# Kernel tuning notes

Hardware: AMD Instinct MI355X
Metric: run time of the kernel (lower is better)

## Reference

```python
import jax, jax.numpy as jnp
import numpy as np

N_NODES = 50000
N_EDGES = 1600000
NODE_DIM = 16
EDGE_DIM = 16
PIPE_F = 4
HID = 64
L = 3


def _lin(k, fan_in, fan_out):
    kw, kb = jax.random.split(k)
    bound = 1.0 / np.sqrt(fan_in)
    w = jax.random.uniform(kw, (fan_in, fan_out), jnp.float32, -bound, bound)
    b = jax.random.uniform(kb, (fan_out,), jnp.float32, -bound, bound)
    return w, b


def setup_inputs() -> dict:
    key = jax.random.key(0)
    ks = jax.random.split(key, 16)
    leak_area = jax.random.normal(ks[0], (N_NODES, 1), jnp.float32)
    pipe_attrs = jax.random.normal(ks[1], (N_EDGES, PIPE_F), jnp.float32)
    edge_index = jax.random.randint(ks[2], (2, N_EDGES), 0, N_NODES, jnp.int32)
    node_embed_w, node_embed_b = _lin(ks[3], 1, NODE_DIM)
    edge_embed_w, edge_embed_b = _lin(ks[4], PIPE_F, EDGE_DIM)
    # per-layer MLP params, stacked along leading layer axis
    ew1, eb1, ew2, eb2, nw1, nb1, nw2, nb2 = [], [], [], [], [], [], [], []
    for l in range(L):
        kl = jax.random.fold_in(ks[5], l)
        k1, k2, k3, k4 = jax.random.split(kl, 4)
        w, b = _lin(k1, 2 * NODE_DIM + EDGE_DIM, HID); ew1.append(w); eb1.append(b)
        w, b = _lin(k2, HID, EDGE_DIM); ew2.append(w); eb2.append(b)
        w, b = _lin(k3, NODE_DIM + EDGE_DIM, HID); nw1.append(w); nb1.append(b)
        w, b = _lin(k4, HID, NODE_DIM); nw2.append(w); nb2.append(b)
    final_node_w, final_node_b = _lin(ks[6], NODE_DIM, 1)
    final_edge_w, final_edge_b = _lin(ks[7], EDGE_DIM, 1)
    return {
        "leak_area": leak_area,
        "pipe_attrs": pipe_attrs,
        "edge_index": edge_index,
        "node_embed_w": node_embed_w, "node_embed_b": node_embed_b,
        "edge_embed_w": edge_embed_w, "edge_embed_b": edge_embed_b,
        "edge_mlp_w1": jnp.stack(ew1), "edge_mlp_b1": jnp.stack(eb1),
        "edge_mlp_w2": jnp.stack(ew2), "edge_mlp_b2": jnp.stack(eb2),
        "node_mlp_w1": jnp.stack(nw1), "node_mlp_b1": jnp.stack(nb1),
        "node_mlp_w2": jnp.stack(nw2), "node_mlp_b2": jnp.stack(nb2),
        "final_node_w": final_node_w, "final_node_b": final_node_b,
        "final_edge_w": final_edge_w, "final_edge_b": final_edge_b,
    }


def reference(leak_area, pipe_attrs, edge_index,
              node_embed_w, node_embed_b, edge_embed_w, edge_embed_b,
              edge_mlp_w1, edge_mlp_b1, edge_mlp_w2, edge_mlp_b2,
              node_mlp_w1, node_mlp_b1, node_mlp_w2, node_mlp_b2,
              final_node_w, final_node_b, final_edge_w, final_edge_b):
    x = leak_area @ node_embed_w + node_embed_b          # [N, node_dim]
    e = pipe_attrs @ edge_embed_w + edge_embed_b          # [E, edge_dim]
    src = edge_index[0]  # x_j (source, PyG default flow source_to_target)
    dst = edge_index[1]  # x_i (target); aggregation index
    n = x.shape[0]
    num_layers = edge_mlp_w1.shape[0]
    ones = jnp.ones((src.shape[0], 1), x.dtype)
    deg = jax.ops.segment_sum(ones, dst, num_segments=n)  # [N,1]
    inv_deg = 1.0 / jnp.maximum(deg, 1.0)
    for l in range(num_layers):
        # message: small MLP on [x_i, x_j, e] per edge
        m_in = jnp.concatenate([x[dst], x[src], e], axis=-1)       # [E, 2d+de]
        h = jax.nn.relu(m_in @ edge_mlp_w1[l] + edge_mlp_b1[l])    # [E, 64]
        msg = h @ edge_mlp_w2[l] + edge_mlp_b2[l]                  # [E, de]
        # mean-aggregate to target nodes
        aggr = jax.ops.segment_sum(msg, dst, num_segments=n) * inv_deg  # [N, de]
        # node update MLP
        u_in = jnp.concatenate([x, aggr], axis=-1)                 # [N, d+de]
        x = jax.nn.relu(u_in @ node_mlp_w1[l] + node_mlp_b1[l]) @ node_mlp_w2[l] + node_mlp_b2[l]
    H = (x @ final_node_w + final_node_b)[:, 0]   # [N]
    q = (e @ final_edge_w + final_edge_b)[:, 0]   # [E]
    return H, q
```

## Files before the change

### kernel.cpp

```cpp
#include <hip/hip_runtime.h>
#include <hip/hip_bf16.h>

#define NN 50000
#define NE 1600000
#define NB 391
#define CBLK 392
#define EPB 4096

typedef __attribute__((ext_vector_type(8))) short bf16x8;
typedef __attribute__((ext_vector_type(4))) float f32x4;

#define B_HAG   0
#define B_QW    (B_HAG + NN*64*4)
#define B_NF    (B_QW + 32)
#define B_W1B   (B_NF + 3*8*64*8*2)
#define B_XB0   (B_W1B + 3*8*64*8*2)
#define B_XB1   (B_XB0 + NN*16*2)
#define B_EPK   (B_XB1 + NN*16*2)
#define B_OFF   (B_EPK + NE*16)
#define B_BCNT  (B_OFF + (NN+1)*4)
#define B_BASE  (B_BCNT + CBLK*NB*4)
#define B_GTOT  (B_BASE + (NB+1)*4)
#define B_END   (B_GTOT + NB*4)

static __device__ __forceinline__ unsigned short f2bf(float f) {
    union { __hip_bfloat16 h; unsigned short u; } cv;
    cv.h = __float2bfloat16(f);
    return cv.u;
}
static __device__ __forceinline__ unsigned pk2(float a, float b) {
    unsigned r;
    asm("v_cvt_pk_bf16_f32 %0, %1, %2" : "=v"(r) : "v"(a), "v"(b));
    return r;
}
static __device__ __forceinline__ float bf2f(unsigned short u) {
    return __uint_as_float((unsigned)u << 16);
}
static __device__ __forceinline__ bf16x8 mk8(unsigned a, unsigned b, unsigned c, unsigned d) {
    union { bf16x8 v; uint4 u; } cv;
    cv.u = make_uint4(a, b, c, d);
    return cv.v;
}

__global__ __launch_bounds__(1024) void fused_init_kernel(
    const float* __restrict__ ew1, const float* __restrict__ eb1,
    const float* __restrict__ nw1, const float* __restrict__ ew2,
    const float* __restrict__ nw2,
    const float* __restrict__ eeW, const float* __restrict__ eeB,
    const float* __restrict__ few, const float* __restrict__ feb,
    unsigned short* __restrict__ w1b, unsigned short* __restrict__ nf,
    float* __restrict__ qw,
    const float* __restrict__ leak, const float* __restrict__ ne_w,
    const float* __restrict__ ne_b,
    unsigned short* __restrict__ xb0, float* __restrict__ hag,
    const int* __restrict__ dst, int* __restrict__ bcnt)
{
    __shared__ int hist[NB];
    int t = threadIdx.x;
    for (int i = t; i < NB; i += 1024) hist[i] = 0;
    __syncthreads();
    int base = blockIdx.x * EPB;
    int b[4];
    #pragma unroll
    for (int i = 0; i < 4; i++) {
        int idx = base + i * 1024 + t;
        b[i] = (idx < NE) ? (dst[idx] >> 7) : -1;
    }
    #pragma unroll
    for (int i = 0; i < 4; i++)
        if (b[i] >= 0) atomicAdd(&hist[b[i]], 1);

    int gtid = blockIdx.x * 1024 + t;
    int gstride = CBLK * 1024;
    for (int idx = gtid; idx < 3 * 8 * 64 * 8; idx += gstride) {
        int l = idx >> 12;
        int r = idx & 4095;
        int f = r >> 9;
        int lane = (r >> 3) & 63;
        int e = r & 7;
        int col = lane & 15;
        int krow = ((lane >> 4) << 3) + e;
        {
            int tt = f >> 1, s = f & 1;
            int k = krow + (s << 5);
            int j = (tt << 4) + col;
            float v = 0.f;
            if (k < 32) {
                v = ew1[l * 3072 + k * 64 + j];
            } else if (k < 36) {
                int f2 = k - 32;
                float acc = 0.f;
                for (int m = 0; m < 16; m++) acc += eeW[f2 * 16 + m] * ew1[l * 3072 + (32 + m) * 64 + j];
                v = acc;
            } else if (k == 36) {
                float acc = eb1[l * 64 + j];
                for (int m = 0; m < 16; m++) acc += eeB[m] * ew1[l * 3072 + (32 + m) * 64 + j];
                v = acc;
            }
            w1b[idx] = f2bf(v);
        }
        {
            float v;
            if (f < 2)      v = ew2[l * 1024 + (f * 32 + krow) * 16 + col];
            else if (f < 6) v = nw1[l * 2048 + krow * 64 + (f - 2) * 16 + col];
            else            v = nw2[l * 1024 + ((f - 6) * 32 + krow) * 16 + col];
            nf[idx] = f2bf(v);
        }
    }
    if (gtid < 4) {
        float s = 0.f;
        for (int k = 0; k < 16; k++) s += eeW[gtid * 16 + k] * few[k];
        qw[gtid] = s;
    } else if (gtid == 4) {
        float s = feb[0];
        for (int k = 0; k < 16; k++) s += eeB[k] * few[k];
        qw[4] = s;
    }
    if (gtid < NN) {
        int n = gtid;
        float la = leak[n];
        float v[16];
        #pragma unroll
        for (int i = 0; i < 16; i++) v[i] = la * ne_w[i] + ne_b[i];
        unsigned pk[8];
        #pragma unroll
        for (int i = 0; i < 8; i++) pk[i] = pk2(v[2 * i], v[2 * i + 1]);
        uint4* xo = reinterpret_cast<uint4*>(xb0 + (size_t)n * 16);
        xo[0] = make_uint4(pk[0], pk[1], pk[2], pk[3]);
        xo[1] = make_uint4(pk[4], pk[5], pk[6], pk[7]);
        float4 z = {0.f, 0.f, 0.f, 0.f};
        float4* hp = reinterpret_cast<float4*>(hag + (size_t)n * 64);
        #pragma unroll
        for (int j = 0; j < 16; j++) hp[j] = z;
    }

    __syncthreads();
    for (int i = t; i < NB; i += 1024) bcnt[blockIdx.x * NB + i] = hist[i];
}

__global__ __launch_bounds__(512) void scan_blocks_kernel(
    int* __restrict__ bcnt, int* __restrict__ gtot)
{
    __shared__ int sm[512];
    int b = blockIdx.x;
    int t = threadIdx.x;
    int v = (t < CBLK) ? bcnt[t * NB + b] : 0;
    sm[t] = v;
    __syncthreads();
    for (int o = 1; o < 512; o <<= 1) {
        int x = (t >= o) ? sm[t - o] : 0;
        __syncthreads();
        sm[t] += x;
        __syncthreads();
    }
    if (t < CBLK) bcnt[t * NB + b] = sm[t] - v;
    if (t == 511) gtot[b] = sm[511];
}

__global__ __launch_bounds__(512) void scan_top_kernel(
    const int* __restrict__ gtot, int* __restrict__ gbase)
{
    __shared__ int sm[512];
    int t = threadIdx.x;
    int v = (t < NB) ? gtot[t] : 0;
    sm[t] = v;
    __syncthreads();
    for (int o = 1; o < 512; o <<= 1) {
        int x = (t >= o) ? sm[t - o] : 0;
        __syncthreads();
        sm[t] += x;
        __syncthreads();
    }
    if (t < NB) gbase[t] = sm[t] - v;
    if (t == 0) gbase[NB] = NE;
}

__global__ __launch_bounds__(1024) void bucket_scatter_kernel(
    const int* __restrict__ ei, const float* __restrict__ pa,
    const int* __restrict__ bcnt, const int* __restrict__ gbase,
    const float* __restrict__ qw,
    float* __restrict__ qout, uint4* __restrict__ epk)
{
    __shared__ int hist[NB];
    int t = threadIdx.x;
    for (int i = t; i < NB; i += 1024) hist[i] = 0;
    __syncthreads();
    int base = blockIdx.x * EPB;
    float q0 = qw[0], q1 = qw[1], q2 = qw[2], q3 = qw[3], q4 = qw[4];
    int d[4], s[4];
    float4 p[4];
    #pragma unroll
    for (int i = 0; i < 4; i++) {
        int idx = base + i * 1024 + t;
        if (idx < NE) {
            d[i] = ei[NE + idx];
            s[i] = ei[idx];
            p[i] = reinterpret_cast<const float4*>(pa)[idx];
        } else {
            d[i] = -1;
        }
    }
    #pragma unroll
    for (int i = 0; i < 4; i++) {
        int idx = base + i * 1024 + t;
        if (d[i] >= 0)
            qout[idx] = q4 + p[i].x * q0 + p[i].y * q1 + p[i].z * q2 + p[i].w * q3;
    }
    int lr[4];
    #pragma unroll
    for (int i = 0; i < 4; i++)
        if (d[i] >= 0) lr[i] = atomicAdd(&hist[d[i] >> 7], 1);
    int bs[4];
    #pragma unroll
    for (int i = 0; i < 4; i++)
        if (d[i] >= 0) {
            int b = d[i] >> 7;
            bs[i] = gbase[b] + bcnt[blockIdx.x * NB + b];
        }
    #pragma unroll
    for (int i = 0; i < 4; i++)
        if (d[i] >= 0) {
            uint4 v;
            v.x = (unsigned)s[i];
            v.y = (unsigned)d[i];
            v.z = pk2(p[i].x, p[i].y);
            v.w = pk2(p[i].z, p[i].w);
            epk[bs[i] + lr[i]] = v;
        }
}

__global__ __launch_bounds__(1024) void fine_sort_kernel(
    const int* __restrict__ gbase, uint4* __restrict__ epk, int* __restrict__ off)
{
    __shared__ int hist[128];
    __shared__ int fb[128];
    int t = threadIdx.x;
    int b = blockIdx.x;
    int S = gbase[b], E = gbase[b + 1];
    if (t < 128) hist[t] = 0;
    __syncthreads();

    uint4 r[12];
    #pragma unroll
    for (int i = 0; i < 12; i++) {
        int gi = S + i * 1024 + t;
        if (gi < E) r[i] = epk[gi];
    }
    int lr[12];
    #pragma unroll
    for (int i = 0; i < 12; i++) {
        int gi = S + i * 1024 + t;
        if (gi < E) lr[i] = atomicAdd(&hist[(int)(r[i].y & 127u)], 1);
    }
    __syncthreads();
    if (t < 128) fb[t] = hist[t];
    __syncthreads();
    for (int o = 1; o < 128; o <<= 1) {
        int v = 0;
        if (t < 128 && t >= o) v = fb[t - o];
        __syncthreads();
        if (t < 128) fb[t] += v;
        __syncthreads();
    }
    int d0 = b << 7;
    if (t < 128 && d0 + t < NN) off[d0 + t] = S + fb[t] - hist[t];
    if (b == NB - 1 && t == 0) off[NN] = NE;
    __syncthreads();
    #pragma unroll
    for (int i = 0; i < 12; i++) {
        int gi = S + i * 1024 + t;
        if (gi < E) {
            int fd = (int)(r[i].y & 127u);
            int pos = S + (fb[fd] - hist[fd]) + lr[i];
            epk[pos] = r[i];
        }
    }
}

__global__ __launch_bounds__(128, 5) void edge_mfma_kernel(
    const unsigned short* __restrict__ xb,
    const uint4* __restrict__ epk,
    const int* __restrict__ off,
    const unsigned short* __restrict__ w1b,
    float* __restrict__ hag)
{
    __shared__ unsigned short hbuf[2][64 * 68];
    int tid = threadIdx.x;
    int lane = tid & 63;
    int wid = tid >> 6;
    int wave = blockIdx.x * 2 + wid;
    int base = wave * 64;
    if (base >= NE) return;
    int ar = lane & 15;
    int ap = lane >> 4;
    unsigned short* hb = &hbuf[wid][0];

    uint4 ev0 = epk[base + 0  + ar];
    uint4 ev1 = epk[base + 16 + ar];
    uint4 ev2 = epk[base + 32 + ar];
    uint4 ev3 = epk[base + 48 + ar];

    int r0 = (ap < 2) ? (int)ev0.y : (int)ev0.x;
    int r1 = (ap < 2) ? (int)ev1.y : (int)ev1.x;
    int r2 = (ap < 2) ? (int)ev2.y : (int)ev2.x;
    int r3 = (ap < 2) ? (int)ev3.y : (int)ev3.x;
    int half = (ap & 1) * 8;
    bf16x8 a00 = *reinterpret_cast<const bf16x8*>(xb + (size_t)r0 * 16 + half);
    bf16x8 a01 = *reinterpret_cast<const bf16x8*>(xb + (size_t)r1 * 16 + half);
    bf16x8 a02 = *reinterpret_cast<const bf16x8*>(xb + (size_t)r2 * 16 + half);
    bf16x8 a03 = *reinterpret_cast<const bf16x8*>(xb + (size_t)r3 * 16 + half);

    int d0 = __builtin_amdgcn_readfirstlane((int)ev0.y);

    bf16x8 Bf[8];
    const bf16x8* w1v = reinterpret_cast<const bf16x8*>(w1b);
    #pragma unroll
    for (int i = 0; i < 8; i++) Bf[i] = w1v[i * 64 + lane];

#define DO_TILE(EV, A0, TILE) do {                                             \
    bf16x8 a1 = (bf16x8)0;                                                     \
    if (ap == 0) {                                                             \
        a1[0] = (short)(EV.z & 0xffffu);                                       \
        a1[1] = (short)(EV.z >> 16);                                           \
        a1[2] = (short)(EV.w & 0xffffu);                                       \
        a1[3] = (short)(EV.w >> 16);                                           \
        a1[4] = (short)0x3f80;                                                 \
    }                                                                          \
    f32x4 C0 = {0.f, 0.f, 0.f, 0.f}, C1 = C0, C2 = C0, C3 = C0;                \
    C0 = __builtin_amdgcn_mfma_f32_16x16x32_bf16(A0, Bf[0], C0, 0, 0, 0);      \
    C0 = __builtin_amdgcn_mfma_f32_16x16x32_bf16(a1, Bf[1], C0, 0, 0, 0);      \
    C1 = __builtin_amdgcn_mfma_f32_16x16x32_bf16(A0, Bf[2], C1, 0, 0, 0);      \
    C1 = __builtin_amdgcn_mfma_f32_16x16x32_bf16(a1, Bf[3], C1, 0, 0, 0);      \
    C2 = __builtin_amdgcn_mfma_f32_16x16x32_bf16(A0, Bf[4], C2, 0, 0, 0);      \
    C2 = __builtin_amdgcn_mfma_f32_16x16x32_bf16(a1, Bf[5], C2, 0, 0, 0);      \
    C3 = __builtin_amdgcn_mfma_f32_16x16x32_bf16(A0, Bf[6], C3, 0, 0, 0);      \
    C3 = __builtin_amdgcn_mfma_f32_16x16x32_bf16(a1, Bf[7], C3, 0, 0, 0);      \
    int eoff = TILE * 16 + ap * 4;                                             \
    {                                                                          \
        unsigned lov = pk2(fmaxf(C0[0], 0.f), fmaxf(C0[1], 0.f));              \
        unsigned hiv = pk2(fmaxf(C0[2], 0.f), fmaxf(C0[3], 0.f));              \
        *reinterpret_cast<uint2*>(hb + (0 * 16 + ar) * 68 + eoff) = make_uint2(lov, hiv); \
    }                                                                          \
    {                                                                          \
        unsigned lov = pk2(fmaxf(C1[0], 0.f), fmaxf(C1[1], 0.f));              \
        unsigned hiv = pk2(fmaxf(C1[2], 0.f), fmaxf(C1[3], 0.f));              \
        *reinterpret_cast<uint2*>(hb + (1 * 16 + ar) * 68 + eoff) = make_uint2(lov, hiv); \
    }                                                                          \
    {                                                                          \
        unsigned lov = pk2(fmaxf(C2[0], 0.f), fmaxf(C2[1], 0.f));              \
        unsigned hiv = pk2(fmaxf(C2[2], 0.f), fmaxf(C2[3], 0.f));              \
        *reinterpret_cast<uint2*>(hb + (2 * 16 + ar) * 68 + eoff) = make_uint2(lov, hiv); \
    }                                                                          \
    {                                                                          \
        unsigned lov = pk2(fmaxf(C3[0], 0.f), fmaxf(C3[1], 0.f));              \
        unsigned hiv = pk2(fmaxf(C3[2], 0.f), fmaxf(C3[3], 0.f));              \
        *reinterpret_cast<uint2*>(hb + (3 * 16 + ar) * 68 + eoff) = make_uint2(lov, hiv); \
    }                                                                          \
} while (0)

    DO_TILE(ev0, a00, 0);
    DO_TILE(ev1, a01, 1);
    DO_TILE(ev2, a02, 2);
    DO_TILE(ev3, a03, 3);
#undef DO_TILE

    asm volatile("s_waitcnt lgkmcnt(0)" ::: "memory");
    __builtin_amdgcn_sched_barrier(0);

    int offd0 = off[d0];
    int d = d0;
    int e = base;
    const int lim = base + 64;
    const unsigned short* hr = hb + lane * 68;
    while (e < lim) {
        int segend = off[d + 1];
        int eend = segend < lim ? segend : lim;
        float acc = 0.f;
        int i = e - base, iend = eend - base;
        for (; (i & 3) != 0 && i < iend; ++i) acc += bf2f(hr[i]);
        for (; i + 4 <= iend; i += 4) {
            uint2 u = *reinterpret_cast<const uint2*>(hr + i);
            acc += __uint_as_float(u.x << 16) + __uint_as_float(u.x & 0xffff0000u)
                 + __uint_as_float(u.y << 16) + __uint_as_float(u.y & 0xffff0000u);
        }
        for (; i < iend; ++i) acc += bf2f(hr[i]);
        bool interior = (segend <= lim) && (e > base || offd0 == base);
        if (interior)
            hag[(size_t)d * 64 + lane] = acc;
        else
            unsafeAtomicAdd(&hag[(size_t)d * 64 + lane], acc);
        e = eend;
        if (segend <= lim) ++d;
    }
}

__global__ __launch_bounds__(256) void node_mfma_kernel(
    const unsigned short* __restrict__ xb, unsigned short* __restrict__ xbn,
    float* __restrict__ hag, const int* __restrict__ off,
    const unsigned short* __restrict__ nf,
    const float* __restrict__ eb2,
    const float* __restrict__ nb1, const float* __restrict__ nb2,
    const float* __restrict__ fnw, const float* __restrict__ fnb,
    float* __restrict__ Hout, int writeH)
{
    __shared__ unsigned short aggt[4][16 * 16];
    __shared__ unsigned short ht[4][16 * 64];
    __shared__ float ot[4][16 * 16];
    int tid = threadIdx.x;
    int lane = tid & 63;
    int wid = tid >> 6;
    int wave = blockIdx.x * 4 + wid;
    int n0 = wave * 16;
    if (n0 >= NN) return;
    int nr = lane & 15;
    int ap = lane >> 4;

    bf16x8 Bf[8];
    const bf16x8* nfv = reinterpret_cast<const bf16x8*>(nf);
    #pragma unroll
    for (int i = 0; i < 8; i++) Bf[i] = nfv[i * 64 + lane];

    float* hrow = hag + (size_t)(n0 + nr) * 64 + ap * 8;
    float4* h0p = reinterpret_cast<float4*>(hrow);
    float4* h1p = reinterpret_cast<float4*>(hrow + 32);
    float4 ha = h0p[0], hc = h0p[1];
    float4 he = h1p[0], hg = h1p[1];
    float4 z = {0.f, 0.f, 0.f, 0.f};
    h0p[0] = z; h0p[1] = z; h1p[0] = z; h1p[1] = z;
    bf16x8 agA0 = mk8(pk2(ha.x, ha.y), pk2(ha.z, ha.w), pk2(hc.x, hc.y), pk2(hc.z, hc.w));
    bf16x8 agA1 = mk8(pk2(he.x, he.y), pk2(he.z, he.w), pk2(hg.x, hg.y), pk2(hg.z, hg.w));
    f32x4 Cag = {0.f, 0.f, 0.f, 0.f};
    Cag = __builtin_amdgcn_mfma_f32_16x16x32_bf16(agA0, Bf[0], Cag, 0, 0, 0);
    Cag = __builtin_amdgcn_mfma_f32_16x16x32_bf16(agA1, Bf[1], Cag, 0, 0, 0);

    int bn = n0 + ap * 4;
    int o0 = off[bn], o1 = off[bn + 1], o2 = off[bn + 2], o3 = off[bn + 3], o4 = off[bn + 4];
    float ebv = eb2[nr];
    {
        int dgs[4] = {o1 - o0, o2 - o1, o3 - o2, o4 - o3};
        #pragma unroll
        for (int r = 0; r < 4; r++) {
            float inv = 1.0f / (float)(dgs[r] > 0 ? dgs[r] : 1);
            float val = Cag[r] * inv + ((dgs[r] > 0) ? ebv : 0.f);
            aggt[wid][(ap * 4 + r) * 16 + nr] = f2bf(val);
        }
    }
    asm volatile("s_waitcnt lgkmcnt(0)" ::: "memory");
    __builtin_amdgcn_sched_barrier(0);

    bf16x8 uA;
    if (ap < 2) uA = *reinterpret_cast<const bf16x8*>(xb + (size_t)(n0 + nr) * 16 + ap * 8);
    else        uA = *reinterpret_cast<const bf16x8*>(&aggt[wid][nr * 16 + (ap - 2) * 8]);

    f32x4 Ch0 = {0.f, 0.f, 0.f, 0.f}, Ch1 = Ch0, Ch2 = Ch0, Ch3 = Ch0;
    Ch0 = __builtin_amdgcn_mfma_f32_16x16x32_bf16(uA, Bf[2], Ch0, 0, 0, 0);
    Ch1 = __builtin_amdgcn_mfma_f32_16x16x32_bf16(uA, Bf[3], Ch1, 0, 0, 0);
    Ch2 = __builtin_amdgcn_mfma_f32_16x16x32_bf16(uA, Bf[4], Ch2, 0, 0, 0);
    Ch3 = __builtin_amdgcn_mfma_f32_16x16x32_bf16(uA, Bf[5], Ch3, 0, 0, 0);

#define H_EPI(C, TT) do {                                                      \
    int j = (TT) * 16 + nr;                                                    \
    float bv = nb1[j];                                                         \
    _Pragma("unroll")                                                          \
    for (int r = 0; r < 4; r++) {                                              \
        float h = fmaxf(C[r] + bv, 0.f);                                       \
        ht[wid][(ap * 4 + r) * 64 + j] = f2bf(h);                              \
    }                                                                          \
} while (0)
    H_EPI(Ch0, 0); H_EPI(Ch1, 1); H_EPI(Ch2, 2); H_EPI(Ch3, 3);
#undef H_EPI

    asm volatile("s_waitcnt lgkmcnt(0)" ::: "memory");
    __builtin_amdgcn_sched_barrier(0);

    bf16x8 hA0 = *reinterpret_cast<const bf16x8*>(&ht[wid][nr * 64 + ap * 8]);
    bf16x8 hA1 = *reinterpret_cast<const bf16x8*>(&ht[wid][nr * 64 + 32 + ap * 8]);
    f32x4 Co = {0.f, 0.f, 0.f, 0.f};
    Co = __builtin_amdgcn_mfma_f32_16x16x32_bf16(hA0, Bf[6], Co, 0, 0, 0);
    Co = __builtin_amdgcn_mfma_f32_16x16x32_bf16(hA1, Bf[7], Co, 0, 0, 0);
    {
        float bv = nb2[nr];
        #pragma unroll
        for (int r = 0; r < 4; r++) ot[wid][(ap * 4 + r) * 16 + nr] = Co[r] + bv;
    }
    asm volatile("s_waitcnt lgkmcnt(0)" ::: "memory");
    __builtin_amdgcn_sched_barrier(0);

    if (lane < 16) {
        const float* orow = &ot[wid][lane * 16];
        float o[16];
        #pragma unroll
        for (int k = 0; k < 16; k++) o[k] = orow[k];
        unsigned pk[8];
        #pragma unroll
        for (int i = 0; i < 8; i++) pk[i] = pk2(o[2 * i], o[2 * i + 1]);
        uint4* xo = reinterpret_cast<uint4*>(xbn + (size_t)(n0 + lane) * 16);
        xo[0] = make_uint4(pk[0], pk[1], pk[2], pk[3]);
        xo[1] = make_uint4(pk[4], pk[5], pk[6], pk[7]);
        if (writeH) {
            float s = fnb[0];
            #pragma unroll
            for (int k = 0; k < 16; k++) s += o[k] * fnw[k];
            Hout[n0 + lane] = s;
        }
    }
}

extern "C" void kernel_launch(void* const* d_in, const int* in_sizes, int n_in,
                              void* d_out, int out_size, void* d_ws, size_t ws_size,
                              hipStream_t stream)
{
    const float* leak = (const float*)d_in[0];
    const float* pa   = (const float*)d_in[1];
    const int*   ei   = (const int*)d_in[2];
    const float* neww = (const float*)d_in[3];
    const float* newb = (const float*)d_in[4];
    const float* eeW  = (const float*)d_in[5];
    const float* eeB  = (const float*)d_in[6];
    const float* ew1  = (const float*)d_in[7];
    const float* eb1  = (const float*)d_in[8];
    const float* ew2  = (const float*)d_in[9];
    const float* eb2  = (const float*)d_in[10];
    const float* nw1  = (const float*)d_in[11];
    const float* nb1  = (const float*)d_in[12];
    const float* nw2  = (const float*)d_in[13];
    const float* nb2  = (const float*)d_in[14];
    const float* fnw  = (const float*)d_in[15];
    const float* fnb  = (const float*)d_in[16];
    const float* few  = (const float*)d_in[17];
    const float* feb  = (const float*)d_in[18];

    char* wsb = (char*)d_ws;
    float*          hag   = (float*)(wsb + B_HAG);
    float*          qw    = (float*)(wsb + B_QW);
    unsigned short* nf    = (unsigned short*)(wsb + B_NF);
    unsigned short* w1b   = (unsigned short*)(wsb + B_W1B);
    unsigned short* xb0   = (unsigned short*)(wsb + B_XB0);
    unsigned short* xb1   = (unsigned short*)(wsb + B_XB1);
    uint4*          epk   = (uint4*)(wsb + B_EPK);
    int*            off   = (int*)(wsb + B_OFF);
    int*            bcnt  = (int*)(wsb + B_BCNT);
    int*            gbase = (int*)(wsb + B_BASE);
    int*            gtot  = (int*)(wsb + B_GTOT);

    float* H = (float*)d_out;
    float* q = (float*)d_out + NN;
    const int* dstp = ei + NE;

    fused_init_kernel<<<CBLK, 1024, 0, stream>>>(
        ew1, eb1, nw1, ew2, nw2, eeW, eeB, few, feb, w1b, nf, qw,
        leak, neww, newb, xb0, hag, dstp, bcnt);
    scan_blocks_kernel<<<NB, 512, 0, stream>>>(bcnt, gtot);
    scan_top_kernel<<<1, 512, 0, stream>>>(gtot, gbase);
    bucket_scatter_kernel<<<CBLK, 1024, 0, stream>>>(ei, pa, bcnt, gbase, qw, q, epk);
    fine_sort_kernel<<<NB, 1024, 0, stream>>>(gbase, epk, off);

    int nwaves = NN / 16;
    int nblocks = (nwaves + 3) / 4;

    unsigned short* xcur = xb0;
    unsigned short* xnxt = xb1;
    for (int l = 0; l < 3; l++) {
        edge_mfma_kernel<<<NE / 128, 128, 0, stream>>>(
            xcur, epk, off, w1b + l * 4096, hag);
        node_mfma_kernel<<<nblocks, 256, 0, stream>>>(
            xcur, xnxt, hag, off, nf + l * 4096, eb2 + l * 16,
            nb1 + l * 64, nb2 + l * 16, fnw, fnb, H, (l == 2) ? 1 : 0);
        unsigned short* tmp = xcur; xcur = xnxt; xnxt = tmp;
    }
}
```

Before: 202.2 us.

## Halve edge-kernel LDS staging by processing two 32-edge halves and raise occupancy

The edge MFMA kernel now stages hidden activations for only 32 edges at a time, cutting per-wave LDS from 64x68 to 64x36 shorts. It runs the segment-sum epilogue twice, once per half, and raises the launch-bounds occupancy hint from 5 to 8 blocks. The aim is more resident waves to hide gather latency. In exchange, every segment write is now an atomic add, including interior ones that were plain stores before, and segments crossing the half boundary produce extra atomics and off[] reads.

```diff
diff --git a/kernel.cpp b/kernel.cpp
--- a/kernel.cpp
+++ b/kernel.cpp
@@ -277,14 +277,14 @@
     }
 }
 
-__global__ __launch_bounds__(128, 5) void edge_mfma_kernel(
+__global__ __launch_bounds__(128, 8) void edge_mfma_kernel(
     const unsigned short* __restrict__ xb,
     const uint4* __restrict__ epk,
     const int* __restrict__ off,
     const unsigned short* __restrict__ w1b,
     float* __restrict__ hag)
 {
-    __shared__ unsigned short hbuf[2][64 * 68];
+    __shared__ unsigned short hbuf[2][64 * 36];
     int tid = threadIdx.x;
     int lane = tid & 63;
     int wid = tid >> 6;
@@ -317,7 +317,7 @@
     #pragma unroll
     for (int i = 0; i < 8; i++) Bf[i] = w1v[i * 64 + lane];
 
-#define DO_TILE(EV, A0, TILE) do {                                             \
+#define DO_TILE(EV, A0, HT) do {                                               \
     bf16x8 a1 = (bf16x8)0;                                                     \
     if (ap == 0) {                                                             \
         a1[0] = (short)(EV.z & 0xffffu);                                       \
@@ -335,63 +335,66 @@
     C2 = __builtin_amdgcn_mfma_f32_16x16x32_bf16(a1, Bf[5], C2, 0, 0, 0);      \
     C3 = __builtin_amdgcn_mfma_f32_16x16x32_bf16(A0, Bf[6], C3, 0, 0, 0);      \
     C3 = __builtin_amdgcn_mfma_f32_16x16x32_bf16(a1, Bf[7], C3, 0, 0, 0);      \
-    int eoff = TILE * 16 + ap * 4;                                             \
+    int eoff = (HT) * 16 + ap * 4;                                             \
     {                                                                          \
         unsigned lov = pk2(fmaxf(C0[0], 0.f), fmaxf(C0[1], 0.f));              \
         unsigned hiv = pk2(fmaxf(C0[2], 0.f), fmaxf(C0[3], 0.f));              \
-        *reinterpret_cast<uint2*>(hb + (0 * 16 + ar) * 68 + eoff) = make_uint2(lov, hiv); \
+        *reinterpret_cast<uint2*>(hb + (0 * 16 + ar) * 36 + eoff) = make_uint2(lov, hiv); \
     }                                                                          \
     {                                                                          \
         unsigned lov = pk2(fmaxf(C1[0], 0.f), fmaxf(C1[1], 0.f));              \
         unsigned hiv = pk2(fmaxf(C1[2], 0.f), fmaxf(C1[3], 0.f));              \
-        *reinterpret_cast<uint2*>(hb + (1 * 16 + ar) * 68 + eoff) = make_uint2(lov, hiv); \
+        *reinterpret_cast<uint2*>(hb + (1 * 16 + ar) * 36 + eoff) = make_uint2(lov, hiv); \
     }                                                                          \
     {                                                                          \
         unsigned lov = pk2(fmaxf(C2[0], 0.f), fmaxf(C2[1], 0.f));              \
         unsigned hiv = pk2(fmaxf(C2[2], 0.f), fmaxf(C2[3], 0.f));              \
-        *reinterpret_cast<uint2*>(hb + (2 * 16 + ar) * 68 + eoff) = make_uint2(lov, hiv); \
+        *reinterpret_cast<uint2*>(hb + (2 * 16 + ar) * 36 + eoff) = make_uint2(lov, hiv); \
     }                                                                          \
     {                                                                          \
         unsigned lov = pk2(fmaxf(C3[0], 0.f), fmaxf(C3[1], 0.f));              \
         unsigned hiv = pk2(fmaxf(C3[2], 0.f), fmaxf(C3[3], 0.f));              \
-        *reinterpret_cast<uint2*>(hb + (3 * 16 + ar) * 68 + eoff) = make_uint2(lov, hiv); \
+        *reinterpret_cast<uint2*>(hb + (3 * 16 + ar) * 36 + eoff) = make_uint2(lov, hiv); \
+    }                                                                          \
+} while (0)
+
+#define EPILOGUE(HSTART, HLIM) do {                                            \
+    const unsigned short* hr = hb + lane * 36;                                 \
+    while (e < (HLIM)) {                                                       \
+        int segend = off[d + 1];                                               \
+        int eend = segend < (HLIM) ? segend : (HLIM);                          \
+        float acc = 0.f;                                                       \
+        int i = e - (HSTART), iend = eend - (HSTART);                          \
+        for (; (i & 3) != 0 && i < iend; ++i) acc += bf2f(hr[i]);              \
+        for (; i + 4 <= iend; i += 4) {                                        \
+            uint2 u = *reinterpret_cast<const uint2*>(hr + i);                 \
+            acc += __uint_as_float(u.x << 16) + __uint_as_float(u.x & 0xffff0000u) \
+                 + __uint_as_float(u.y << 16) + __uint_as_float(u.y & 0xffff0000u); \
+        }                                                                      \
+        for (; i < iend; ++i) acc += bf2f(hr[i]);                              \
+        unsafeAtomicAdd(&hag[(size_t)d * 64 + lane], acc);                     \
+        e = eend;                                                              \
+        if (segend <= (HLIM)) ++d;                                             \
     }                                                                          \
 } while (0)
 
     DO_TILE(ev0, a00, 0);
     DO_TILE(ev1, a01, 1);
-    DO_TILE(ev2, a02, 2);
-    DO_TILE(ev3, a03, 3);
-#undef DO_TILE
-
     asm volatile("s_waitcnt lgkmcnt(0)" ::: "memory");
     __builtin_amdgcn_sched_barrier(0);
-
-    int offd0 = off[d0];
     int d = d0;
     int e = base;
-    const int lim = base + 64;
-    const unsigned short* hr = hb + lane * 68;
-    while (e < lim) {
-        int segend = off[d + 1];
-        int eend = segend < lim ? segend : lim;
-        float acc = 0.f;
-        int i = e - base, iend = eend - base;
-        for (; (i & 3) != 0 && i < iend; ++i) acc += bf2f(hr[i]);
-        for (; i + 4 <= iend; i += 4) {
-            uint2 u = *reinterpret_cast<const uint2*>(hr + i);
-            acc += __uint_as_float(u.x << 16) + __uint_as_float(u.x & 0xffff0000u)
-                 + __uint_as_float(u.y << 16) + __uint_as_float(u.y & 0xffff0000u);
-        }
-        for (; i < iend; ++i) acc += bf2f(hr[i]);
-        bool interior = (segend <= lim) && (e > base || offd0 == base);
-        if (interior)
-            hag[(size_t)d * 64 + lane] = acc;
-        else
-            unsafeAtomicAdd(&hag[(size_t)d * 64 + lane], acc);
-        e = eend;
-        if (segend <= lim) ++d;
-    }
+    EPILOGUE(base, base + 32);
+    asm volatile("s_waitcnt lgkmcnt(0)" ::: "memory");
+    __builtin_amdgcn_sched_barrier(0);
+
+    DO_TILE(ev2, a02, 0);
+    DO_TILE(ev3, a03, 1);
+    asm volatile("s_waitcnt lgkmcnt(0)" ::: "memory");
+    __builtin_amdgcn_sched_barrier(0);
+    EPILOGUE(base + 32, base + 64);
+#undef DO_TILE
+#undef EPILOGUE
 }
 
 __global__ __launch_bounds__(256) void node_mfma_kernel(
```

Result: slower. 571.7 us (+182.7%).
